# Performance work log

Measured on AMD Instinct MI355X. Metric: run time of the kernel, lower is better.

The kernel has to match this reference:

```python
import jax, jax.numpy as jnp
import numpy as np

B, N, M, H = 16, 2048, 512, 512

def setup_inputs() -> dict:
    key = jax.random.key(0)
    ks = jax.random.split(key, 12)
    s_m = 1.0 / np.sqrt(M)
    s_h = 1.0 / np.sqrt(H)
    return {
        "d": jax.random.uniform(ks[0], (B, N), dtype=jnp.float32),
        "h": jax.random.normal(ks[1], (B, N, M), dtype=jnp.float32),
        "Wv": jax.random.normal(ks[2], (M, H), dtype=jnp.float32) * s_m,
        "bv": jnp.zeros((H,), jnp.float32),
        "Wk": jax.random.normal(ks[3], (M, H), dtype=jnp.float32) * s_m,
        "bk": jnp.full((H,), 0.01, jnp.float32),
        "Wq": jax.random.normal(ks[4], (M, H), dtype=jnp.float32) * s_m,
        "bq": jnp.zeros((H,), jnp.float32),
        "W1": jax.random.normal(ks[5], (H, H), dtype=jnp.float32) * s_h,
        "b1": jnp.zeros((H,), jnp.float32),
        "W2": jax.random.normal(ks[6], (H, M), dtype=jnp.float32) * s_h,
        "b2": jnp.zeros((M,), jnp.float32),
    }

def reference(d, h, Wv, bv, Wk, bk, Wq, bq, W1, b1, W2, b2):
    # d is unused by the original forward
    v = h @ Wv + bv                      # [B, N, H]
    q = h @ Wq + bq                      # [B, N, H]
    k = h @ Wk + bk                      # [B, N, H]
    att = jnp.einsum('bnh,bmh->bnm', q, k)   # [B, N, N]  (no 1/sqrt scaling, as in source)
    att = jax.nn.softmax(att, axis=-1)
    out = jnp.einsum('bnm,bmh->bnh', att, v)  # [B, N, H]
    hid = jax.nn.relu(out @ W1 + b1)
    return hid @ W2 + b2                 # [B, N, M]
```

## Files before the change

### kernel.cpp

```cpp
#include <hip/hip_runtime.h>
#include <cstdint>
#include <cstddef>

typedef _Float16 f16;
typedef __attribute__((ext_vector_type(8))) _Float16 f16x8;
typedef __attribute__((ext_vector_type(4))) _Float16 f16x4;
typedef __attribute__((ext_vector_type(4))) float f32x4;

#define AS1 const __attribute__((address_space(1))) void*
#define AS3 __attribute__((address_space(3))) void*

__device__ __forceinline__ void gld_lds16(const void* g, void* l) {
    __builtin_amdgcn_global_load_lds((AS1)g, (AS3)l, 16, 0, 0);
}

__global__ __launch_bounds__(256) void prep_weights(
    const float* __restrict__ Wv, const float* __restrict__ Wk, const float* __restrict__ Wq,
    const float* __restrict__ W1, const float* __restrict__ W2,
    const float* __restrict__ bq, const float* __restrict__ bk, const float* __restrict__ bv,
    f16* __restrict__ Wqkv_h, f16* __restrict__ Wqkv_l,
    f16* __restrict__ W1t, f16* __restrict__ W2t, float* __restrict__ bias_qkv) {
    int i = blockIdx.x * 256 + threadIdx.x;
    if (i < 1536 * 512) {
        int j = i >> 9, m = i & 511;
        float w = (j < 512) ? Wq[m * 512 + j]
               : (j < 1024) ? Wk[m * 512 + (j - 512)]
                            : Wv[m * 512 + (j - 1024)];
        f16 hi = (f16)w;
        Wqkv_h[i] = hi;
        Wqkv_l[i] = (f16)(w - (float)hi);
    }
    if (i < 512 * 512) {
        int j = i >> 9, m = i & 511;
        W1t[i] = (f16)W1[m * 512 + j];
        W2t[i] = (f16)W2[m * 512 + j];
    }
    if (i < 1536) {
        bias_qkv[i] = (i < 512) ? bq[i] : (i < 1024) ? bk[i - 512] : bv[i - 1024];
    }
}

enum { MODE_QKV = 0, MODE_S = 1, MODE_PV = 2, MODE_HID = 3, MODE_FIN = 4 };

template <int MODE, int TN>
__global__ __launch_bounds__(256, 2) void gemm_nt(
    const void* __restrict__ Av, const f16* __restrict__ Alp, int lda, long long sA,
    const f16* __restrict__ Bp, const f16* __restrict__ Blp, int ldb, long long sB,
    void* __restrict__ C, int ldc, long long sC,
    const float* __restrict__ bias, int K,
    f16* __restrict__ Qh, f16* __restrict__ Ql,
    f16* __restrict__ Kh, f16* __restrict__ Kl, f16* __restrict__ Vt)
{
    constexpr bool AF32 = (MODE == MODE_QKV);
    constexpr bool SPA  = (MODE == MODE_S);
    constexpr bool SPB  = (MODE == MODE_QKV || MODE == MODE_S);
    constexpr int ABYTES = AF32 ? 128 * 32 * 4 : 128 * 32 * 2;
    constexpr int BBYTES = TN * 32 * 2;
    constexpr int NA = SPA ? 2 : 1;
    constexpr int NB = SPB ? 2 : 1;
    constexpr int NW = TN / 32;
    __shared__ alignas(16) char lds[2][NA * ABYTES + NB * BBYTES];

    const int lane = threadIdx.x & 63;
    const int wave = threadIdx.x >> 6;
    const int z = blockIdx.z;

    const float* A32 = (const float*)Av;
    const f16* A = (const f16*)Av + (long long)z * sA;
    const f16* Al = nullptr;
    if constexpr (SPA) Al = Alp + (long long)z * sA;
    const f16* B = Bp + (long long)z * sB;
    const f16* Bl = nullptr;
    if constexpr (SPB) Bl = Blp + (long long)z * sB;
    char* Cb = (char*)C + (long long)z * sC;

    const int rowBase = blockIdx.y * 128;
    const int colBase = blockIdx.x * TN;

    auto stage = [&](int buf, int kt) {
        char* base = lds[buf];
        const int k0 = kt << 5;
        if constexpr (AF32) {
            const int segr = lane >> 3;
            const int segk = (lane & 7) * 4;
            #pragma unroll
            for (int c = 0; c < 4; ++c) {
                const int seg = wave * 4 + c;
                const int r = seg * 8 + segr;
                gld_lds16(A32 + (size_t)(rowBase + r) * lda + k0 + segk,
                          base + seg * 1024);
            }
        } else {
            const int segr = lane >> 2;
            const int segk = (lane & 3) * 8;
            #pragma unroll
            for (int c = 0; c < 2; ++c) {
                const int seg = wave * 2 + c;
                const int r = seg * 16 + segr;
                const size_t off = (size_t)(rowBase + r) * lda + k0 + segk;
                gld_lds16(A + off, base + seg * 1024);
                if constexpr (SPA) gld_lds16(Al + off, base + ABYTES + seg * 1024);
            }
        }
        {
            char* bb = lds[buf] + NA * ABYTES;
            const int segr = lane >> 2;
            const int segk = (lane & 3) * 8;
            constexpr int CB = TN / 64;
            #pragma unroll
            for (int c = 0; c < CB; ++c) {
                const int seg = wave * CB + c;
                const int r = seg * 16 + segr;
                const size_t off = (size_t)(colBase + r) * ldb + k0 + segk;
                gld_lds16(B + off, bb + seg * 1024);
                if constexpr (SPB) gld_lds16(Bl + off, bb + BBYTES + seg * 1024);
            }
        }
    };

    f32x4 acc[4][NW] = {};
    const int nK = K >> 5;
    stage(0, 0);

    const int wr = wave >> 1, wc = wave & 1;
    const int cl = lane & 15;
    const int kq = lane >> 4;
    const int kofs = kq * 8;

    for (int kt = 0; kt < nK; ++kt) {
        const int buf = kt & 1;
        __syncthreads();
        if (kt + 1 < nK) stage(buf ^ 1, kt + 1);

        f16x8 ah[4], alo[4], bh[NW], blo[NW];
        const char* bufp = lds[buf];
        if constexpr (AF32) {
            #pragma unroll
            for (int m = 0; m < 4; ++m) {
                const float* ap = (const float*)bufp + (wr * 64 + m * 16 + cl) * 32 + kofs;
                const f32x4 u = *(const f32x4*)ap;
                const f32x4 w = *(const f32x4*)(ap + 4);
                #pragma unroll
                for (int j = 0; j < 4; ++j) {
                    f16 h0 = (f16)u[j]; ah[m][j] = h0; alo[m][j] = (f16)(u[j] - (float)h0);
                    f16 h1 = (f16)w[j]; ah[m][4 + j] = h1; alo[m][4 + j] = (f16)(w[j] - (float)h1);
                }
            }
        } else {
            #pragma unroll
            for (int m = 0; m < 4; ++m) {
                const int eo = ((wr * 64 + m * 16 + cl) * 32 + kofs) * 2;
                ah[m] = *(const f16x8*)(bufp + eo);
                if constexpr (SPA) alo[m] = *(const f16x8*)(bufp + ABYTES + eo);
            }
        }
        {
            const char* bb = bufp + NA * ABYTES;
            #pragma unroll
            for (int n = 0; n < NW; ++n) {
                const int eo = ((wc * (TN / 2) + n * 16 + cl) * 32 + kofs) * 2;
                bh[n] = *(const f16x8*)(bb + eo);
                if constexpr (SPB) blo[n] = *(const f16x8*)(bb + BBYTES + eo);
            }
        }
        #pragma unroll
        for (int m = 0; m < 4; ++m)
            #pragma unroll
            for (int n = 0; n < NW; ++n) {
                acc[m][n] = __builtin_amdgcn_mfma_f32_16x16x32_f16(ah[m], bh[n], acc[m][n], 0, 0, 0);
                if constexpr (SPB)
                    acc[m][n] = __builtin_amdgcn_mfma_f32_16x16x32_f16(ah[m], blo[n], acc[m][n], 0, 0, 0);
                if constexpr (AF32 || SPA)
                    acc[m][n] = __builtin_amdgcn_mfma_f32_16x16x32_f16(alo[m], bh[n], acc[m][n], 0, 0, 0);
            }
    }

    #pragma unroll
    for (int m = 0; m < 4; ++m) {
        #pragma unroll
        for (int n = 0; n < NW; ++n) {
            const f32x4 a = acc[m][n];
            const int col = colBase + wc * (TN / 2) + n * 16 + cl;
            float bval = 0.f;
            if constexpr (MODE == MODE_QKV || MODE == MODE_HID || MODE == MODE_FIN)
                bval = bias[col];
            #pragma unroll
            for (int j = 0; j < 4; ++j) {
                const int row = rowBase + wr * 64 + m * 16 + kq * 4 + j;
                const float v = a[j] + bval;
                if constexpr (MODE == MODE_S) {
                    ((float*)Cb)[(size_t)row * ldc + col] = v;
                } else if constexpr (MODE == MODE_PV) {
                    ((f16*)Cb)[(size_t)row * ldc + col] = (f16)v;
                } else if constexpr (MODE == MODE_HID) {
                    ((f16*)Cb)[(size_t)row * ldc + col] = (f16)fmaxf(v, 0.f);
                } else if constexpr (MODE == MODE_FIN) {
                    ((float*)Cb)[(size_t)row * ldc + col] = v;
                } else {
                    if (col < 1024) {
                        const f16 hi = (f16)v;
                        const f16 lo = (f16)(v - (float)hi);
                        const size_t idx = (size_t)row * 512 + (col & 511);
                        if (col < 512) { Qh[idx] = hi; Ql[idx] = lo; }
                        else           { Kh[idx] = hi; Kl[idx] = lo; }
                    } else {
                        Vt[((size_t)(row >> 11) * 512 + (col - 1024)) * 2048 + (row & 2047)] = (f16)v;
                    }
                }
            }
        }
    }
}

__global__ __launch_bounds__(256) void softmax_rows(float* __restrict__ S) {
    const int wave = threadIdx.x >> 6, lane = threadIdx.x & 63;
    float* rp = S + ((size_t)blockIdx.x * 4 + wave) * 2048;
    f32x4 v[8];
    float mx = -3.0e38f;
    #pragma unroll
    for (int s = 0; s < 8; ++s) {
        v[s] = ((const f32x4*)rp)[s * 64 + lane];
        mx = fmaxf(mx, fmaxf(fmaxf(v[s][0], v[s][1]), fmaxf(v[s][2], v[s][3])));
    }
    #pragma unroll
    for (int off = 32; off; off >>= 1) mx = fmaxf(mx, __shfl_xor(mx, off));
    float sum = 0.f;
    #pragma unroll
    for (int s = 0; s < 8; ++s)
        #pragma unroll
        for (int j = 0; j < 4; ++j) { const float e = __expf(v[s][j] - mx); v[s][j] = e; sum += e; }
    #pragma unroll
    for (int off = 32; off; off >>= 1) sum += __shfl_xor(sum, off);
    const float inv = 1.0f / sum;
    f16* op = (f16*)rp;
    #pragma unroll
    for (int s = 0; s < 8; ++s) {
        f16x4 o;
        #pragma unroll
        for (int j = 0; j < 4; ++j) o[j] = (f16)(v[s][j] * inv);
        ((f16x4*)op)[s * 64 + lane] = o;
    }
}

extern "C" void kernel_launch(void* const* d_in, const int* in_sizes, int n_in,
                              void* d_out, int out_size, void* d_ws, size_t ws_size,
                              hipStream_t stream) {
    const float* h  = (const float*)d_in[1];
    const float* Wv = (const float*)d_in[2];
    const float* bv = (const float*)d_in[3];
    const float* Wk = (const float*)d_in[4];
    const float* bk = (const float*)d_in[5];
    const float* Wq = (const float*)d_in[6];
    const float* bq = (const float*)d_in[7];
    const float* W1 = (const float*)d_in[8];
    const float* b1 = (const float*)d_in[9];
    const float* W2 = (const float*)d_in[10];
    const float* b2 = (const float*)d_in[11];

    char* p = (char*)d_ws;
    auto take = [&](size_t bytes) { char* r = p; p += (bytes + 255) & ~(size_t)255; return r; };

    const size_t QB = (size_t)32768 * 512 * 2;
    f16* qh = (f16*)take(QB);
    f16* ql = (f16*)take(QB);
    f16* kh = (f16*)take(QB);
    f16* kl = (f16*)take(QB);
    f16* vt = (f16*)take(QB);
    float* S = (float*)take((size_t)2 * 2048 * 2048 * 4);
    f16* Wqkvh = (f16*)take(1536 * 512 * 2);
    f16* Wqkvl = (f16*)take(1536 * 512 * 2);
    f16* W1t   = (f16*)take(512 * 512 * 2);
    f16* W2t   = (f16*)take(512 * 512 * 2);
    float* biasqkv = (float*)take(1536 * 4);
    f16* outb = kl;
    f16* hid  = qh;

    prep_weights<<<3072, 256, 0, stream>>>(Wv, Wk, Wq, W1, W2, bq, bk, bv,
                                           Wqkvh, Wqkvl, W1t, W2t, biasqkv);
    gemm_nt<MODE_QKV, 128><<<dim3(12, 256, 1), 256, 0, stream>>>(
        h, nullptr, 512, 0, Wqkvh, Wqkvl, 512, 0,
        nullptr, 0, 0, biasqkv, 512, qh, ql, kh, kl, vt);

    for (int c = 0; c < 8; ++c) {
        const long long off = (long long)c * 2 * 2048 * 512;
        gemm_nt<MODE_S, 128><<<dim3(16, 16, 2), 256, 0, stream>>>(
            qh + off, ql + off, 512, 1048576LL,
            kh + off, kl + off, 512, 1048576LL,
            S, 2048, 16777216LL, nullptr, 512,
            nullptr, nullptr, nullptr, nullptr, nullptr);
        softmax_rows<<<1024, 256, 0, stream>>>(S);
        gemm_nt<MODE_PV, 64><<<dim3(8, 16, 2), 256, 0, stream>>>(
            (const f16*)S, nullptr, 4096, 8388608LL,
            vt + off, nullptr, 2048, 1048576LL,
            outb + off, 512, 2097152LL, nullptr, 2048,
            nullptr, nullptr, nullptr, nullptr, nullptr);
    }

    gemm_nt<MODE_HID, 128><<<dim3(4, 256, 1), 256, 0, stream>>>(
        outb, nullptr, 512, 0, W1t, nullptr, 512, 0,
        hid, 512, 0, b1, 512, nullptr, nullptr, nullptr, nullptr, nullptr);
    gemm_nt<MODE_FIN, 128><<<dim3(4, 256, 1), 256, 0, stream>>>(
        hid, nullptr, 512, 0, W2t, nullptr, 512, 0,
        d_out, 512, 0, b2, 512, nullptr, nullptr, nullptr, nullptr, nullptr);
}
```

Before: 952.6 us.

## Pre-cast h to f16 and run split-precision GEMMs as concatenated K segments

A new kernel casts the fp32 input h to f16 once, ahead of the GEMMs. The QKV GEMM then reads f16 A and drops the h-low correction term, keeping only the weight hi/lo split. The GEMM kernel is generalised so that split-precision products (hi*hi, lo*hi, hi*lo) become a K loop over up to three pointer segments, which shrinks LDS use and register arrays. Tile M sizes and the occupancy hint are also retuned for the S and PV GEMMs. This removes the in-loop fp32-to-f16 conversion and a third of the QKV MFMAs, at the cost of lower accuracy in the Q/K/V projections.

```diff
diff --git a/kernel.cpp b/kernel.cpp
--- a/kernel.cpp
+++ b/kernel.cpp
@@ -12,6 +12,17 @@
 
 __device__ __forceinline__ void gld_lds16(const void* g, void* l) {
     __builtin_amdgcn_global_load_lds((AS1)g, (AS3)l, 16, 0, 0);
+}
+
+__global__ __launch_bounds__(256) void cast_h(const float* __restrict__ in,
+                                              f16* __restrict__ hh, int n4) {
+    int i = blockIdx.x * 256 + threadIdx.x;
+    if (i >= n4) return;
+    f32x4 x = ((const f32x4*)in)[i];
+    f16x4 a;
+    #pragma unroll
+    for (int j = 0; j < 4; ++j) a[j] = (f16)x[j];
+    ((f16x4*)hh)[i] = a;
 }
 
 __global__ __launch_bounds__(256) void prep_weights(
@@ -42,84 +53,66 @@
 
 enum { MODE_QKV = 0, MODE_S = 1, MODE_PV = 2, MODE_HID = 3, MODE_FIN = 4 };
 
-template <int MODE, int TN>
-__global__ __launch_bounds__(256, 2) void gemm_nt(
-    const void* __restrict__ Av, const f16* __restrict__ Alp, int lda, long long sA,
-    const f16* __restrict__ Bp, const f16* __restrict__ Blp, int ldb, long long sB,
+template <int MODE, int TM, int TN, int NSEG>
+__global__ __launch_bounds__(256, 4) void gemm_nt(
+    const f16* __restrict__ A0, const f16* __restrict__ A1, const f16* __restrict__ A2,
+    int lda, long long sA,
+    const f16* __restrict__ B0, const f16* __restrict__ B1, const f16* __restrict__ B2,
+    int ldb, long long sB,
     void* __restrict__ C, int ldc, long long sC,
-    const float* __restrict__ bias, int K,
+    const float* __restrict__ bias, int nK,
     f16* __restrict__ Qh, f16* __restrict__ Ql,
     f16* __restrict__ Kh, f16* __restrict__ Kl, f16* __restrict__ Vt)
 {
-    constexpr bool AF32 = (MODE == MODE_QKV);
-    constexpr bool SPA  = (MODE == MODE_S);
-    constexpr bool SPB  = (MODE == MODE_QKV || MODE == MODE_S);
-    constexpr int ABYTES = AF32 ? 128 * 32 * 4 : 128 * 32 * 2;
+    constexpr int ABYTES = TM * 32 * 2;
     constexpr int BBYTES = TN * 32 * 2;
-    constexpr int NA = SPA ? 2 : 1;
-    constexpr int NB = SPB ? 2 : 1;
+    constexpr int MF = TM / 32;
     constexpr int NW = TN / 32;
-    __shared__ alignas(16) char lds[2][NA * ABYTES + NB * BBYTES];
+    constexpr int AISS = TM / 64;
+    constexpr int BISS = TN / 64;
+    __shared__ alignas(16) char lds[2][ABYTES + BBYTES];
 
     const int lane = threadIdx.x & 63;
     const int wave = threadIdx.x >> 6;
     const int z = blockIdx.z;
 
-    const float* A32 = (const float*)Av;
-    const f16* A = (const f16*)Av + (long long)z * sA;
-    const f16* Al = nullptr;
-    if constexpr (SPA) Al = Alp + (long long)z * sA;
-    const f16* B = Bp + (long long)z * sB;
-    const f16* Bl = nullptr;
-    if constexpr (SPB) Bl = Blp + (long long)z * sB;
+    const f16* a0 = A0 + (long long)z * sA;
+    const f16* a1 = A1 + (long long)z * sA;
+    const f16* a2 = A2 + (long long)z * sA;
+    const f16* b0 = B0 + (long long)z * sB;
+    const f16* b1 = B1 + (long long)z * sB;
+    const f16* b2 = B2 + (long long)z * sB;
     char* Cb = (char*)C + (long long)z * sC;
 
-    const int rowBase = blockIdx.y * 128;
+    const int rowBase = blockIdx.y * TM;
     const int colBase = blockIdx.x * TN;
 
+    const int segr = lane >> 2;
+    const int segk = (lane & 3) * 8;
+
     auto stage = [&](int buf, int kt) {
+        int seg, k0;
+        if constexpr (NSEG > 1) { seg = kt >> 4; k0 = (kt & 15) << 5; }
+        else                    { seg = 0;       k0 = kt << 5; }
+        const f16* Ap = (seg == 0) ? a0 : (seg == 1 ? a1 : a2);
+        const f16* Bp = (seg == 0) ? b0 : (seg == 1 ? b1 : b2);
         char* base = lds[buf];
-        const int k0 = kt << 5;
-        if constexpr (AF32) {
-            const int segr = lane >> 3;
-            const int segk = (lane & 7) * 4;
-            #pragma unroll
-            for (int c = 0; c < 4; ++c) {
-                const int seg = wave * 4 + c;
-                const int r = seg * 8 + segr;
-                gld_lds16(A32 + (size_t)(rowBase + r) * lda + k0 + segk,
-                          base + seg * 1024);
-            }
-        } else {
-            const int segr = lane >> 2;
-            const int segk = (lane & 3) * 8;
-            #pragma unroll
-            for (int c = 0; c < 2; ++c) {
-                const int seg = wave * 2 + c;
-                const int r = seg * 16 + segr;
-                const size_t off = (size_t)(rowBase + r) * lda + k0 + segk;
-                gld_lds16(A + off, base + seg * 1024);
-                if constexpr (SPA) gld_lds16(Al + off, base + ABYTES + seg * 1024);
-            }
+        #pragma unroll
+        for (int c = 0; c < AISS; ++c) {
+            const int sg = wave * AISS + c;
+            const int r = sg * 16 + segr;
+            gld_lds16(Ap + (size_t)(rowBase + r) * lda + k0 + segk, base + sg * 1024);
         }
-        {
-            char* bb = lds[buf] + NA * ABYTES;
-            const int segr = lane >> 2;
-            const int segk = (lane & 3) * 8;
-            constexpr int CB = TN / 64;
-            #pragma unroll
-            for (int c = 0; c < CB; ++c) {
-                const int seg = wave * CB + c;
-                const int r = seg * 16 + segr;
-                const size_t off = (size_t)(colBase + r) * ldb + k0 + segk;
-                gld_lds16(B + off, bb + seg * 1024);
-                if constexpr (SPB) gld_lds16(Bl + off, bb + BBYTES + seg * 1024);
-            }
+        #pragma unroll
+        for (int c = 0; c < BISS; ++c) {
+            const int sg = wave * BISS + c;
+            const int r = sg * 16 + segr;
+            gld_lds16(Bp + (size_t)(colBase + r) * ldb + k0 + segk,
+                      base + ABYTES + sg * 1024);
         }
     };
 
-    f32x4 acc[4][NW] = {};
-    const int nK = K >> 5;
+    f32x4 acc[MF][NW] = {};
     stage(0, 0);
 
     const int wr = wave >> 1, wc = wave & 1;
@@ -132,51 +125,23 @@
         __syncthreads();
         if (kt + 1 < nK) stage(buf ^ 1, kt + 1);
 
-        f16x8 ah[4], alo[4], bh[NW], blo[NW];
+        f16x8 ah[MF], bh[NW];
         const char* bufp = lds[buf];
-        if constexpr (AF32) {
+        #pragma unroll
+        for (int m = 0; m < MF; ++m)
+            ah[m] = *(const f16x8*)(bufp + ((wr * (TM / 2) + m * 16 + cl) * 32 + kofs) * 2);
+        #pragma unroll
+        for (int n = 0; n < NW; ++n)
+            bh[n] = *(const f16x8*)(bufp + ABYTES + ((wc * (TN / 2) + n * 16 + cl) * 32 + kofs) * 2);
+        #pragma unroll
+        for (int m = 0; m < MF; ++m)
             #pragma unroll
-            for (int m = 0; m < 4; ++m) {
-                const float* ap = (const float*)bufp + (wr * 64 + m * 16 + cl) * 32 + kofs;
-                const f32x4 u = *(const f32x4*)ap;
-                const f32x4 w = *(const f32x4*)(ap + 4);
-                #pragma unroll
-                for (int j = 0; j < 4; ++j) {
-                    f16 h0 = (f16)u[j]; ah[m][j] = h0; alo[m][j] = (f16)(u[j] - (float)h0);
-                    f16 h1 = (f16)w[j]; ah[m][4 + j] = h1; alo[m][4 + j] = (f16)(w[j] - (float)h1);
-                }
-            }
-        } else {
-            #pragma unroll
-            for (int m = 0; m < 4; ++m) {
-                const int eo = ((wr * 64 + m * 16 + cl) * 32 + kofs) * 2;
-                ah[m] = *(const f16x8*)(bufp + eo);
-                if constexpr (SPA) alo[m] = *(const f16x8*)(bufp + ABYTES + eo);
-            }
-        }
-        {
-            const char* bb = bufp + NA * ABYTES;
-            #pragma unroll
-            for (int n = 0; n < NW; ++n) {
-                const int eo = ((wc * (TN / 2) + n * 16 + cl) * 32 + kofs) * 2;
-                bh[n] = *(const f16x8*)(bb + eo);
-                if constexpr (SPB) blo[n] = *(const f16x8*)(bb + BBYTES + eo);
-            }
-        }
-        #pragma unroll
-        for (int m = 0; m < 4; ++m)
-            #pragma unroll
-            for (int n = 0; n < NW; ++n) {
+            for (int n = 0; n < NW; ++n)
                 acc[m][n] = __builtin_amdgcn_mfma_f32_16x16x32_f16(ah[m], bh[n], acc[m][n], 0, 0, 0);
-                if constexpr (SPB)
-                    acc[m][n] = __builtin_amdgcn_mfma_f32_16x16x32_f16(ah[m], blo[n], acc[m][n], 0, 0, 0);
-                if constexpr (AF32 || SPA)
-                    acc[m][n] = __builtin_amdgcn_mfma_f32_16x16x32_f16(alo[m], bh[n], acc[m][n], 0, 0, 0);
-            }
-    }
-
-    #pragma unroll
-    for (int m = 0; m < 4; ++m) {
+    }
+
+    #pragma unroll
+    for (int m = 0; m < MF; ++m) {
         #pragma unroll
         for (int n = 0; n < NW; ++n) {
             const f32x4 a = acc[m][n];
@@ -186,7 +151,7 @@
                 bval = bias[col];
             #pragma unroll
             for (int j = 0; j < 4; ++j) {
-                const int row = rowBase + wr * 64 + m * 16 + kq * 4 + j;
+                const int row = rowBase + wr * (TM / 2) + m * 16 + kq * 4 + j;
                 const float v = a[j] + bval;
                 if constexpr (MODE == MODE_S) {
                     ((float*)Cb)[(size_t)row * ldc + col] = v;
@@ -272,34 +237,37 @@
     f16* W1t   = (f16*)take(512 * 512 * 2);
     f16* W2t   = (f16*)take(512 * 512 * 2);
     float* biasqkv = (float*)take(1536 * 4);
+    f16* hh   = (f16*)S;
     f16* outb = kl;
     f16* hid  = qh;
 
+    cast_h<<<16384, 256, 0, stream>>>(h, hh, 4194304);
     prep_weights<<<3072, 256, 0, stream>>>(Wv, Wk, Wq, W1, W2, bq, bk, bv,
                                            Wqkvh, Wqkvl, W1t, W2t, biasqkv);
-    gemm_nt<MODE_QKV, 128><<<dim3(12, 256, 1), 256, 0, stream>>>(
-        h, nullptr, 512, 0, Wqkvh, Wqkvl, 512, 0,
-        nullptr, 0, 0, biasqkv, 512, qh, ql, kh, kl, vt);
+    gemm_nt<MODE_QKV, 128, 128, 2><<<dim3(12, 256, 1), 256, 0, stream>>>(
+        hh, hh, nullptr, 512, 0,
+        Wqkvh, Wqkvl, nullptr, 512, 0,
+        nullptr, 0, 0, biasqkv, 32, qh, ql, kh, kl, vt);
 
     for (int c = 0; c < 8; ++c) {
         const long long off = (long long)c * 2 * 2048 * 512;
-        gemm_nt<MODE_S, 128><<<dim3(16, 16, 2), 256, 0, stream>>>(
-            qh + off, ql + off, 512, 1048576LL,
-            kh + off, kl + off, 512, 1048576LL,
-            S, 2048, 16777216LL, nullptr, 512,
+        gemm_nt<MODE_S, 64, 128, 3><<<dim3(16, 32, 2), 256, 0, stream>>>(
+            qh + off, ql + off, qh + off, 512, 1048576LL,
+            kh + off, kh + off, kl + off, 512, 1048576LL,
+            S, 2048, 16777216LL, nullptr, 48,
             nullptr, nullptr, nullptr, nullptr, nullptr);
         softmax_rows<<<1024, 256, 0, stream>>>(S);
-        gemm_nt<MODE_PV, 64><<<dim3(8, 16, 2), 256, 0, stream>>>(
-            (const f16*)S, nullptr, 4096, 8388608LL,
-            vt + off, nullptr, 2048, 1048576LL,
-            outb + off, 512, 2097152LL, nullptr, 2048,
+        gemm_nt<MODE_PV, 64, 64, 1><<<dim3(8, 32, 2), 256, 0, stream>>>(
+            (const f16*)S, nullptr, nullptr, 4096, 8388608LL,
+            vt + off, nullptr, nullptr, 2048, 1048576LL,
+            outb + off, 512, 2097152LL, nullptr, 64,
             nullptr, nullptr, nullptr, nullptr, nullptr);
     }
 
-    gemm_nt<MODE_HID, 128><<<dim3(4, 256, 1), 256, 0, stream>>>(
-        outb, nullptr, 512, 0, W1t, nullptr, 512, 0,
-        hid, 512, 0, b1, 512, nullptr, nullptr, nullptr, nullptr, nullptr);
-    gemm_nt<MODE_FIN, 128><<<dim3(4, 256, 1), 256, 0, stream>>>(
-        hid, nullptr, 512, 0, W2t, nullptr, 512, 0,
-        d_out, 512, 0, b2, 512, nullptr, nullptr, nullptr, nullptr, nullptr);
-}
+    gemm_nt<MODE_HID, 128, 128, 1><<<dim3(4, 256, 1), 256, 0, stream>>>(
+        outb, nullptr, nullptr, 512, 0, W1t, nullptr, nullptr, 512, 0,
+        hid, 512, 0, b1, 16, nullptr, nullptr, nullptr, nullptr, nullptr);
+    gemm_nt<MODE_FIN, 128, 128, 1><<<dim3(4, 256, 1), 256, 0, stream>>>(
+        hid, nullptr, nullptr, 512, 0, W2t, nullptr, nullptr, 512, 0,
+        d_out, 512, 0, b2, 16, nullptr, nullptr, nullptr, nullptr, nullptr);
+}
```

After: 1.793 ms. 88.2% more time.
